# Kernel tuning notes

Hardware: AMD Instinct MI355X
Metric: run time of the kernel (lower is better)

The kernel has to match this reference:

```python
import jax, jax.numpy as jnp
import numpy as np

# pywt db4 decomposition filters (dec_lo, dec_hi), 8 taps
DEC_LO = np.array([-0.010597401784997278, 0.032883011666982945, 0.030841381835986965,
                   -0.18703481171888114, -0.02798376941698385, 0.6308807679295904,
                   0.7148465705525415, 0.23037781330885523])
DEC_HI = np.array([-0.23037781330885523, 0.7148465705525415, -0.6308807679295904,
                   -0.02798376941698385, 0.18703481171888114, 0.030841381835986965,
                   -0.032883011666982945, -0.010597401784997278])
HEADS = 8


def dwt_db4(v):
    # Equivalent of pywt.dwt(v, 'db4') (mode='symmetric') applied along last axis.
    # Symmetric (half-point) extension by L-1=7, full convolution, downsample taking
    # every 2nd sample starting at conv index 1 -> out_len = floor((n+7)/2).
    pad = [(0, 0)] * (v.ndim - 1) + [(7, 7)]
    ext = jnp.pad(v, pad, mode='symmetric')[..., 1:]
    lead = v.shape[:-1]
    lhs = ext.reshape(-1, 1, ext.shape[-1])                       # (N, 1, n+13)
    rhs = jnp.stack([jnp.asarray(DEC_LO[::-1], v.dtype),
                     jnp.asarray(DEC_HI[::-1], v.dtype)])[:, None, :]  # (2, 1, 8)
    out = jax.lax.conv_general_dilated(lhs, rhs, (2,), 'VALID')   # (N, 2, out_len)
    out = out.reshape(*lead, 2, -1)
    return out[..., 0, :], out[..., 1, :]


def setup_inputs() -> dict:
    key = jax.random.key(0)
    k0, k1, k2, k3 = jax.random.split(key, 4)
    B, S, H = 4, 2048, 1024
    a = float(np.sqrt(6.0 / (H + H)))  # xavier_uniform bound
    x = jax.random.normal(k0, (B, S, H), dtype=jnp.float32)
    Wq = jax.random.uniform(k1, (H, H), jnp.float32, -a, a)
    Wk = jax.random.uniform(k2, (H, H), jnp.float32, -a, a)
    Wv = jax.random.uniform(k3, (H, H), jnp.float32, -a, a)
    return {"x": x, "Wq": Wq, "Wk": Wk, "Wv": Wv}


def reference(x, Wq, Wk, Wv):
    B, S, Hd = x.shape
    H = HEADS
    dk = Hd // H
    scale = dk ** -0.5
    # torch nn.Linear: y = x @ W.T
    q = (x @ Wq.T).reshape(B, S, H, dk).transpose(0, 2, 1, 3) * scale  # (B,H,S,dk)
    k = (x @ Wk.T).reshape(B, S, H, dk).transpose(0, 2, 1, 3)
    v = (x @ Wv.T).reshape(B, S, H, dk).transpose(0, 2, 1, 3)
    attn = jax.nn.softmax(jnp.einsum('bhqd,bhkd->bhqk', q, k), axis=-1)
    cA, cD = dwt_db4(v)                                   # (B,H,S,wA) each
    wA = cA.shape[-1]
    wcD = jnp.einsum('bhqk,bhkw->bhqw', attn, cD)
    out1 = wcD.transpose(0, 2, 1, 3).reshape(B, S, H * wA)
    out2 = cA.reshape(-1, S, H * wA)                      # faithful raw view of (B,H,S,wA)
    return out1, out2
```

## Files before the change

### kernel.cpp

```cpp
#include <hip/hip_runtime.h>
#include <hip/hip_bf16.h>

#define B_ 4
#define S_ 2048
#define HD 1024
#define NH 8
#define DK 128
#define WA 67
#define WPAD 80

typedef __attribute__((ext_vector_type(8))) short short8;
typedef __attribute__((ext_vector_type(4))) short short4v;
typedef __attribute__((ext_vector_type(4))) float floatx4;

__device__ __forceinline__ float hexp2(float x) { return __builtin_amdgcn_exp2f(x); }

__device__ __forceinline__ short f2bf(float f) {
    union { float f; unsigned u; } c; c.f = f;
    unsigned u = c.u;
    u += 0x7FFF + ((u >> 16) & 1);
    return (short)(u >> 16);
}
__device__ __forceinline__ float bf2f(short s) {
    union { unsigned u; float f; } c; c.u = ((unsigned)(unsigned short)s) << 16;
    return c.f;
}
__device__ __forceinline__ short f2bf_trunc(float f) {
    union { float f; unsigned u; } c; c.f = f;
    return (short)(c.u >> 16);
}

__device__ __forceinline__ void glds16(void* lds, const void* g) {
    __builtin_amdgcn_global_load_lds(
        (const __attribute__((address_space(1))) unsigned*)g,
        (__attribute__((address_space(3))) unsigned*)lds, 16, 0, 0);
}

__device__ __constant__ float FLO[8] = {
    0.23037781330885523f,  0.7148465705525415f,  0.6308807679295904f,
   -0.02798376941698385f, -0.18703481171888114f, 0.030841381835986965f,
    0.032883011666982945f, -0.010597401784997278f };
__device__ __constant__ float FHI[8] = {
   -0.010597401784997278f, -0.032883011666982945f, 0.030841381835986965f,
    0.18703481171888114f,  -0.02798376941698385f, -0.6308807679295904f,
    0.7148465705525415f,   -0.23037781330885523f };

__global__ __launch_bounds__(256) void cvt_all(
    const float* __restrict__ x,  const float* __restrict__ wq,
    const float* __restrict__ wk, const float* __restrict__ wv,
    short* __restrict__ xb, short* __restrict__ wb)
{
    const size_t w_elems = (size_t)HD * HD;
    int blk = blockIdx.x;
    const float* src; short* dst; int lb;
    if (blk < 4096)      { src = x;  dst = xb;               lb = blk; }
    else if (blk < 4608) { src = wq; dst = wb;               lb = blk - 4096; }
    else if (blk < 5120) { src = wk; dst = wb + w_elems;     lb = blk - 4608; }
    else                 { src = wv; dst = wb + 2 * w_elems; lb = blk - 5120; }
    int i = lb * 256 + threadIdx.x;
    const float4* s = (const float4*)src + (size_t)i * 2;
    float4 f0 = s[0], f1 = s[1];
    short8 o;
    o[0] = f2bf(f0.x); o[1] = f2bf(f0.y); o[2] = f2bf(f0.z); o[3] = f2bf(f0.w);
    o[4] = f2bf(f1.x); o[5] = f2bf(f1.y); o[6] = f2bf(f1.z); o[7] = f2bf(f1.w);
    *((short8*)dst + i) = o;
}

__global__ __launch_bounds__(512) void qkv_gemm(
    const short* __restrict__ xb, const short* __restrict__ Wb,
    short* __restrict__ Qb, short* __restrict__ Kb,
    float* __restrict__ outA, short* __restrict__ cdt)
{
    __shared__ __align__(16) short Asb[3][256 * 64];
    __shared__ __align__(16) short Bsb[3][128 * 64];
    const int tid  = threadIdx.x;
    const int wid  = tid >> 6;
    const int lane = tid & 63;
    const int l15  = lane & 15;
    const int quad = lane >> 4;
    const int rx   = l15 & 7;
    const int wm   = wid >> 1;
    const int wn   = wid & 1;
    const int m0 = blockIdx.x * 256;
    const int by = blockIdx.y;
    const int z  = by >> 3;
    const int n0 = (by & 7) * 128;
    const short* W = Wb + (size_t)z * HD * HD;
    const float scale = (z == 0) ? 0.12751743786072596f : 1.0f;
    const int srow = lane >> 3;
    const int sch  = (lane & 7) ^ srow;

    floatx4 acc[4][4] = {};

    auto stA = [&](int bf, int t) {
        #pragma unroll
        for (int i = 0; i < 4; ++i) {
            int ti = wid * 4 + i;
            glds16(&Asb[bf][ti * 512],
                   xb + (size_t)(m0 + ti * 8 + srow) * HD + t * 64 + sch * 8);
        }
    };
    auto stB = [&](int bf, int t) {
        #pragma unroll
        for (int i = 0; i < 2; ++i) {
            int ti = wid * 2 + i;
            glds16(&Bsb[bf][ti * 512],
                   W + (size_t)(n0 + ti * 8 + srow) * HD + t * 64 + sch * 8);
        }
    };

#define VM6 asm volatile("s_waitcnt vmcnt(6)" ::: "memory")
#define VM0 asm volatile("s_waitcnt vmcnt(0)" ::: "memory")
#define BARRIER do { asm volatile("" ::: "memory"); \
                     __builtin_amdgcn_s_barrier(); \
                     asm volatile("" ::: "memory"); } while (0)

    stA(0, 0); stB(0, 0);
    stA(1, 1); stB(1, 1);
    VM6; BARRIER;

    #pragma unroll
    for (int t = 0; t < 16; ++t) {
        const int cur = t % 3;
        const int sb  = (t + 2) % 3;
        {
            short8 af[4], bf4[4];
            #pragma unroll
            for (int mt = 0; mt < 4; ++mt)
                af[mt] = *(const short8*)
                    &Asb[cur][(wm * 64 + mt * 16 + l15) * 64 + ((quad ^ rx) * 8)];
            #pragma unroll
            for (int nt = 0; nt < 4; ++nt)
                bf4[nt] = *(const short8*)
                    &Bsb[cur][(wn * 64 + nt * 16 + l15) * 64 + ((quad ^ rx) * 8)];
            if (t < 14) stA(sb, t + 2);
            BARRIER;
            __builtin_amdgcn_s_setprio(1);
            #pragma unroll
            for (int mt = 0; mt < 4; ++mt)
                #pragma unroll
                for (int nt = 0; nt < 4; ++nt)
                    acc[mt][nt] = __builtin_amdgcn_mfma_f32_16x16x32_bf16(
                        af[mt], bf4[nt], acc[mt][nt], 0, 0, 0);
            __builtin_amdgcn_s_setprio(0);
            BARRIER;
        }
        {
            short8 af[4], bf4[4];
            #pragma unroll
            for (int mt = 0; mt < 4; ++mt)
                af[mt] = *(const short8*)
                    &Asb[cur][(wm * 64 + mt * 16 + l15) * 64 + (((4 + quad) ^ rx) * 8)];
            #pragma unroll
            for (int nt = 0; nt < 4; ++nt)
                bf4[nt] = *(const short8*)
                    &Bsb[cur][(wn * 64 + nt * 16 + l15) * 64 + (((4 + quad) ^ rx) * 8)];
            if (t < 14) stB(sb, t + 2);
            if (t < 14) { VM6; } else if (t == 14) { VM0; }
            BARRIER;
            __builtin_amdgcn_s_setprio(1);
            #pragma unroll
            for (int mt = 0; mt < 4; ++mt)
                #pragma unroll
                for (int nt = 0; nt < 4; ++nt)
                    acc[mt][nt] = __builtin_amdgcn_mfma_f32_16x16x32_bf16(
                        af[mt], bf4[nt], acc[mt][nt], 0, 0, 0);
            __builtin_amdgcn_s_setprio(0);
            BARRIER;
        }
    }
    __syncthreads();

    if (z != 2) {
        short* Yb = (z == 0) ? Qb : Kb;
        #pragma unroll
        for (int mt = 0; mt < 4; ++mt)
            #pragma unroll
            for (int nt = 0; nt < 4; ++nt)
                #pragma unroll
                for (int reg = 0; reg < 4; ++reg) {
                    int rg = m0 + wm * 64 + mt * 16 + quad * 4 + reg;
                    int cg = n0 + wn * 64 + nt * 16 + l15;
                    int b = rg >> 11, s = rg & 2047;
                    int h = cg >> 7,  d = cg & 127;
                    Yb[((size_t)(b * NH + h) * S_ + s) * DK + d] =
                        f2bf(acc[mt][nt][reg] * scale);
                }
        return;
    }
    short* Cs = &Asb[0][0];
    #pragma unroll
    for (int mt = 0; mt < 4; ++mt)
        #pragma unroll
        for (int nt = 0; nt < 4; ++nt)
            #pragma unroll
            for (int reg = 0; reg < 4; ++reg) {
                int r = wm * 64 + mt * 16 + quad * 4 + reg;
                int c = wn * 64 + nt * 16 + l15;
                Cs[r * 130 + c] = f2bf(acc[mt][nt][reg]);
            }
    __syncthreads();
    const int rl    = tid & 255;
    const int chunk = tid >> 8;
    const int rg = m0 + rl;
    const int b = rg >> 11, s = rg & 2047;
    const int bh = b * NH + (by & 7);
    const short* vr = Cs + rl * 130;
    auto getv = [&](int i) -> float {
        int k = (i < 6) ? (5 - i) : (i < 134) ? (i - 6) : (261 - i);
        return bf2f(vr[k]);
    };
    const int t0 = chunk * 34;
    const int t1 = (chunk == 0) ? 34 : WA;
    float win[8];
    #pragma unroll
    for (int j = 0; j < 8; ++j) win[j] = getv(2 * t0 + j);
    float* oA = outA + ((size_t)bh * S_ + s) * WA;
    for (int t = t0; t < t1; ++t) {
        float lo = 0.f, hi = 0.f;
        #pragma unroll
        for (int j = 0; j < 8; ++j) { lo += win[j] * FLO[j]; hi += win[j] * FHI[j]; }
        oA[t] = lo;
        cdt[((size_t)bh * WPAD + t) * S_ + s] = f2bf(hi);
        #pragma unroll
        for (int j = 0; j < 6; ++j) win[j] = win[j + 2];
        if (t + 1 < t1) { win[6] = getv(2 * t + 8); win[7] = getv(2 * t + 9); }
    }
    if (chunk == 1) {
        #pragma unroll
        for (int w = WA; w < WPAD; ++w)
            cdt[((size_t)bh * WPAD + w) * S_ + s] =
                (w == 67) ? (short)0x3F80 : (short)0;
    }
#undef BARRIER
#undef VM6
#undef VM0
}

__global__ __launch_bounds__(256, 2) void attn_kernel(
    const short* __restrict__ Qb, const short* __restrict__ Kb,
    const short* __restrict__ cdt, float* __restrict__ out1)
{
    __shared__ __align__(16) short Ks[64 * 128];
    __shared__ __align__(16) short Ds[WPAD * 64];
    __shared__ __align__(16) short Pt[8 * 1024];
    const int tid  = threadIdx.x;
    const int wv   = tid >> 6;
    const int lane = tid & 63;
    const int l15  = lane & 15;
    const int quad = lane >> 4;
    const int qt = blockIdx.x;
    const int bh = blockIdx.y;
    const int b = bh >> 3, h = bh & 7;
    const int rxor = l15 & 7;

    short8 aq[2][4];
    #pragma unroll
    for (int n = 0; n < 2; ++n) {
        const short* qrow =
            Qb + ((size_t)bh * S_ + qt * 128 + wv * 32 + n * 16 + l15) * DK;
        #pragma unroll
        for (int s4 = 0; s4 < 4; ++s4)
            aq[n][s4] = *(const short8*)(qrow + s4 * 32 + quad * 8);
    }

    floatx4 O[2][5] = {};

    const short* kbase = Kb + (size_t)bh * S_ * DK;
    const int krow = lane >> 4;
    const int kch  = (lane & 15);
    const int drow = lane >> 3;
    const int dch  = (lane & 7) ^ (drow & 7);
    short* ptw = Pt + wv * 2048;

    for (int kt = 0; kt < 32; ++kt) {
        __syncthreads();
        #pragma unroll
        for (int i = 0; i < 4; ++i) {
            int ti = wv * 4 + i;
            int r  = ti * 4 + krow;
            int ch = kch ^ (r & 7);
            glds16(Ks + ti * 512, kbase + ((size_t)kt * 64 + r) * DK + ch * 8);
        }
        #pragma unroll
        for (int i = 0; i < 3; ++i) {
            int t = wv + i * 4;
            if (t < 10) {
                int r = t * 8 + drow;
                glds16(Ds + t * 512,
                       cdt + ((size_t)bh * WPAD + r) * S_ + kt * 64 + dch * 8);
            }
        }
        __syncthreads();

        floatx4 sc[2][4] = {};
        #pragma unroll
        for (int s4 = 0; s4 < 4; ++s4) {
            short8 kf[4];
            #pragma unroll
            for (int mt = 0; mt < 4; ++mt) {
                int ch = (s4 * 4 + quad) ^ rxor;
                kf[mt] = *(const short8*)&Ks[(mt * 16 + l15) * 128 + ch * 8];
            }
            #pragma unroll
            for (int n = 0; n < 2; ++n)
                #pragma unroll
                for (int mt = 0; mt < 4; ++mt)
                    sc[n][mt] = __builtin_amdgcn_mfma_f32_16x16x32_bf16(
                        kf[mt], aq[n][s4], sc[n][mt], 0, 0, 0);
        }
        #pragma unroll
        for (int n = 0; n < 2; ++n) {
            #pragma unroll
            for (int mt = 0; mt < 4; ++mt) {
                short4v pk;
                #pragma unroll
                for (int reg = 0; reg < 4; ++reg)
                    pk[reg] = f2bf_trunc(hexp2(sc[n][mt][reg]));
                int ch = (mt * 2 + (quad >> 1)) ^ rxor;
                *(short4v*)&ptw[n * 1024 + l15 * 64 + ch * 8 + (quad & 1) * 4] = pk;
            }
        }
        short8 ap[2][2];
        #pragma unroll
        for (int mt = 0; mt < 2; ++mt)
            #pragma unroll
            for (int ks = 0; ks < 2; ++ks) {
                int ch = (ks * 4 + quad) ^ rxor;
                ap[mt][ks] = *(const short8*)&ptw[mt * 1024 + l15 * 64 + ch * 8];
            }
        #pragma unroll
        for (int j = 0; j < 5; ++j) {
            #pragma unroll
            for (int ks = 0; ks < 2; ++ks) {
                int ch = (ks * 4 + quad) ^ rxor;
                short8 bd = *(const short8*)&Ds[(j * 16 + l15) * 64 + ch * 8];
                #pragma unroll
                for (int mt = 0; mt < 2; ++mt)
                    O[mt][j] = __builtin_amdgcn_mfma_f32_16x16x32_bf16(
                        ap[mt][ks], bd, O[mt][j], 0, 0, 0);
            }
        }
    }
    float rl[2][4];
    #pragma unroll
    for (int mt = 0; mt < 2; ++mt)
        #pragma unroll
        for (int reg = 0; reg < 4; ++reg)
            rl[mt][reg] = 1.0f / __shfl(O[mt][4][reg], (quad << 4) | 3, 64);
    #pragma unroll
    for (int mt = 0; mt < 2; ++mt)
        #pragma unroll
        for (int j = 0; j < 5; ++j) {
            int w = j * 16 + l15;
            if (w < WA) {
                #pragma unroll
                for (int reg = 0; reg < 4; ++reg) {
                    int qrow_g = qt * 128 + wv * 32 + mt * 16 + quad * 4 + reg;
                    out1[((size_t)(b * S_ + qrow_g)) * (NH * WA) + h * WA + w] =
                        O[mt][j][reg] * rl[mt][reg];
                }
            }
        }
}

extern "C" void kernel_launch(void* const* d_in, const int* in_sizes, int n_in,
                              void* d_out, int out_size, void* d_ws, size_t ws_size,
                              hipStream_t stream)
{
    const float* x  = (const float*)d_in[0];
    const float* Wq = (const float*)d_in[1];
    const float* Wk = (const float*)d_in[2];
    const float* Wv = (const float*)d_in[3];
    float* out = (float*)d_out;

    const size_t x_elems   = (size_t)B_ * S_ * HD;
    const size_t w_elems   = (size_t)HD * HD;
    const size_t qkv_elems = (size_t)B_ * NH * S_ * DK;
    short* xb  = (short*)d_ws;
    short* Wb  = xb + x_elems;
    short* Qb  = Wb + 3 * w_elems;
    short* Kb  = Qb + qkv_elems;
    short* cdt = Kb + qkv_elems;
    float* out1 = out;
    float* out2 = out + (size_t)B_ * S_ * NH * WA;

    cvt_all<<<dim3(5632), 256, 0, stream>>>(x, Wq, Wk, Wv, xb, Wb);
    qkv_gemm<<<dim3(32, 24), 512, 0, stream>>>(xb, Wb, Qb, Kb, out2, cdt);
    attn_kernel<<<dim3(16, 32), 256, 0, stream>>>(Qb, Kb, cdt, out1);
}
```

Measured before the change: 233.8 us.

## Shrink QKV GEMM tile to 128x128 with double buffering for two blocks per CU

The QKV projection GEMM moves from 512-thread blocks with 256x128 tiles and triple buffering to 256-thread blocks with 128x128 tiles and a simple double buffer. Each iteration prefetches the next K-slice and then waits with vmcnt(0) and a single barrier, replacing the finer-grained split-wait schedule. The grid doubles along M and the launch bound asks for two blocks per CU, so more blocks can share a CU to hide latency. In exchange each tile reuses less data, and the full wait each step may expose global load latency that the three-stage pipeline used to hide.

```diff
diff --git a/kernel.cpp b/kernel.cpp
--- a/kernel.cpp
+++ b/kernel.cpp
@@ -66,13 +66,12 @@
     *((short8*)dst + i) = o;
 }
 
-__global__ __launch_bounds__(512) void qkv_gemm(
+__global__ __launch_bounds__(256, 2) void qkv_gemm(
     const short* __restrict__ xb, const short* __restrict__ Wb,
     short* __restrict__ Qb, short* __restrict__ Kb,
     float* __restrict__ outA, short* __restrict__ cdt)
 {
-    __shared__ __align__(16) short Asb[3][256 * 64];
-    __shared__ __align__(16) short Bsb[3][128 * 64];
+    __shared__ __align__(16) short SM[32768];
     const int tid  = threadIdx.x;
     const int wid  = tid >> 6;
     const int lane = tid & 63;
@@ -81,7 +80,7 @@
     const int rx   = l15 & 7;
     const int wm   = wid >> 1;
     const int wn   = wid & 1;
-    const int m0 = blockIdx.x * 256;
+    const int m0 = blockIdx.x * 128;
     const int by = blockIdx.y;
     const int z  = by >> 3;
     const int n0 = (by & 7) * 128;
@@ -92,49 +91,52 @@
 
     floatx4 acc[4][4] = {};
 
+    auto Abuf = [&](int bf) -> short* { return SM + bf * 8192; };
+    auto Bbuf = [&](int bf) -> short* { return SM + 16384 + bf * 8192; };
+
     auto stA = [&](int bf, int t) {
+        short* d = Abuf(bf);
         #pragma unroll
         for (int i = 0; i < 4; ++i) {
             int ti = wid * 4 + i;
-            glds16(&Asb[bf][ti * 512],
+            glds16(d + ti * 512,
                    xb + (size_t)(m0 + ti * 8 + srow) * HD + t * 64 + sch * 8);
         }
     };
     auto stB = [&](int bf, int t) {
-        #pragma unroll
-        for (int i = 0; i < 2; ++i) {
-            int ti = wid * 2 + i;
-            glds16(&Bsb[bf][ti * 512],
+        short* d = Bbuf(bf);
+        #pragma unroll
+        for (int i = 0; i < 4; ++i) {
+            int ti = wid * 4 + i;
+            glds16(d + ti * 512,
                    W + (size_t)(n0 + ti * 8 + srow) * HD + t * 64 + sch * 8);
         }
     };
 
-#define VM6 asm volatile("s_waitcnt vmcnt(6)" ::: "memory")
 #define VM0 asm volatile("s_waitcnt vmcnt(0)" ::: "memory")
 #define BARRIER do { asm volatile("" ::: "memory"); \
                      __builtin_amdgcn_s_barrier(); \
                      asm volatile("" ::: "memory"); } while (0)
 
     stA(0, 0); stB(0, 0);
-    stA(1, 1); stB(1, 1);
-    VM6; BARRIER;
-
-    #pragma unroll
+    VM0; BARRIER;
+
     for (int t = 0; t < 16; ++t) {
-        const int cur = t % 3;
-        const int sb  = (t + 2) % 3;
-        {
+        const int cur = t & 1, nxt = cur ^ 1;
+        if (t < 15) { stA(nxt, t + 1); stB(nxt, t + 1); }
+        const short* Ab = Abuf(cur);
+        const short* Bb = Bbuf(cur);
+        #pragma unroll
+        for (int ks = 0; ks < 2; ++ks) {
             short8 af[4], bf4[4];
             #pragma unroll
             for (int mt = 0; mt < 4; ++mt)
                 af[mt] = *(const short8*)
-                    &Asb[cur][(wm * 64 + mt * 16 + l15) * 64 + ((quad ^ rx) * 8)];
+                    &Ab[(wm * 64 + mt * 16 + l15) * 64 + (((ks * 4 + quad) ^ rx) * 8)];
             #pragma unroll
             for (int nt = 0; nt < 4; ++nt)
                 bf4[nt] = *(const short8*)
-                    &Bsb[cur][(wn * 64 + nt * 16 + l15) * 64 + ((quad ^ rx) * 8)];
-            if (t < 14) stA(sb, t + 2);
-            BARRIER;
+                    &Bb[(wn * 64 + nt * 16 + l15) * 64 + (((ks * 4 + quad) ^ rx) * 8)];
             __builtin_amdgcn_s_setprio(1);
             #pragma unroll
             for (int mt = 0; mt < 4; ++mt)
@@ -143,33 +145,10 @@
                     acc[mt][nt] = __builtin_amdgcn_mfma_f32_16x16x32_bf16(
                         af[mt], bf4[nt], acc[mt][nt], 0, 0, 0);
             __builtin_amdgcn_s_setprio(0);
-            BARRIER;
-        }
-        {
-            short8 af[4], bf4[4];
-            #pragma unroll
-            for (int mt = 0; mt < 4; ++mt)
-                af[mt] = *(const short8*)
-                    &Asb[cur][(wm * 64 + mt * 16 + l15) * 64 + (((4 + quad) ^ rx) * 8)];
-            #pragma unroll
-            for (int nt = 0; nt < 4; ++nt)
-                bf4[nt] = *(const short8*)
-                    &Bsb[cur][(wn * 64 + nt * 16 + l15) * 64 + (((4 + quad) ^ rx) * 8)];
-            if (t < 14) stB(sb, t + 2);
-            if (t < 14) { VM6; } else if (t == 14) { VM0; }
-            BARRIER;
-            __builtin_amdgcn_s_setprio(1);
-            #pragma unroll
-            for (int mt = 0; mt < 4; ++mt)
-                #pragma unroll
-                for (int nt = 0; nt < 4; ++nt)
-                    acc[mt][nt] = __builtin_amdgcn_mfma_f32_16x16x32_bf16(
-                        af[mt], bf4[nt], acc[mt][nt], 0, 0, 0);
-            __builtin_amdgcn_s_setprio(0);
-            BARRIER;
-        }
-    }
-    __syncthreads();
+        }
+        VM0;
+        BARRIER;
+    }
 
     if (z != 2) {
         short* Yb = (z == 0) ? Qb : Kb;
@@ -188,7 +167,7 @@
                 }
         return;
     }
-    short* Cs = &Asb[0][0];
+    short* Cs = SM;
     #pragma unroll
     for (int mt = 0; mt < 4; ++mt)
         #pragma unroll
@@ -200,8 +179,8 @@
                 Cs[r * 130 + c] = f2bf(acc[mt][nt][reg]);
             }
     __syncthreads();
-    const int rl    = tid & 255;
-    const int chunk = tid >> 8;
+    const int rl    = tid & 127;
+    const int chunk = tid >> 7;
     const int rg = m0 + rl;
     const int b = rg >> 11, s = rg & 2047;
     const int bh = b * NH + (by & 7);
@@ -233,7 +212,6 @@
                 (w == 67) ? (short)0x3F80 : (short)0;
     }
 #undef BARRIER
-#undef VM6
 #undef VM0
 }
 
@@ -386,6 +364,6 @@
     float* out2 = out + (size_t)B_ * S_ * NH * WA;
 
     cvt_all<<<dim3(5632), 256, 0, stream>>>(x, Wq, Wk, Wv, xb, Wb);
-    qkv_gemm<<<dim3(32, 24), 512, 0, stream>>>(xb, Wb, Qb, Kb, out2, cdt);
+    qkv_gemm<<<dim3(64, 24), 256, 0, stream>>>(xb, Wb, Qb, Kb, out2, cdt);
     attn_kernel<<<dim3(16, 32), 256, 0, stream>>>(Qb, Kb, cdt, out1);
 }
```

Measured after the change: 222.3 us. 4.9% less time.
